# Kernel optimization log

Measured on AMD Instinct MI355X. Metric: run time of the kernel, lower is better.

## Reference

```python
import jax, jax.numpy as jnp
import numpy as np

CLAMP_MIN = -1.0
CLAMP_MAX = 1.0
EPS = 1e-5


def setup_inputs() -> dict:
    key = jax.random.key(0)
    k1, k2, k3, k4 = jax.random.split(key, 4)
    x = jax.random.normal(k1, (16, 3, 64, 64, 64), dtype=jnp.float32)
    w = jax.random.normal(k2, (16, 3, 3, 3, 3), dtype=jnp.float32) * 0.11  # ~kaiming scale for fan_in=81
    b = jax.random.normal(k3, (16,), dtype=jnp.float32) * 0.1
    m = jax.random.normal(k4, (16, 1, 1, 1), dtype=jnp.float32)
    return {"x": x, "w": w, "b": b, "m": m}


def reference(x, w, b, m):
    # Valid 3D conv: [N,3,D,H,W] x [16,3,3,3,3] -> [N,16,D-2,H-2,W-2]
    y = jax.lax.conv_general_dilated(
        x, w, window_strides=(1, 1, 1), padding='VALID',
        dimension_numbers=('NCDHW', 'OIDHW', 'NCDHW'))
    y = y + b[None, :, None, None, None]
    y = y * m[None]  # per-channel multiply before instance norm
    # InstanceNorm3d (affine=False, biased variance) over spatial dims per (n, c)
    mu = jnp.mean(y, axis=(2, 3, 4), keepdims=True)
    var = jnp.var(y, axis=(2, 3, 4), keepdims=True)
    y = (y - mu) * jax.lax.rsqrt(var + EPS)
    # clamp, second per-channel multiply, then max over channel dim
    y = jnp.clip(y, CLAMP_MIN, CLAMP_MAX) * m[None]
    return jnp.max(y, axis=1)  # [N, D-2, H-2, W-2]
```

## Files before the change

### kernel.cpp

```cpp
#include <hip/hip_runtime.h>
#include <hip/hip_bf16.h>
#include <float.h>

#define DI   64
#define DOUT 62
#define CI   3
#define CO   16
#define NB   16
constexpr int SP    = DOUT * DOUT * DOUT;
constexpr int SP64  = DOUT * DOUT * 64;
constexpr int HT    = 31;
constexpr int DT    = 16;
constexpr int NPART = HT * DT;
constexpr int XDW   = NB * CI * DI * DI * DI / 2;
constexpr int RSTR  = 34;
constexpr int PHD   = 72 * RSTR;

typedef __attribute__((ext_vector_type(8))) short bf16x8;
typedef __attribute__((ext_vector_type(4))) float f32x4;

__device__ float g_psum[NB * CO * NPART];
__device__ float g_psq [NB * CO * NPART];
__device__ float g_stats[NB * CO * 2];
__device__ uint4 g_wb4[4 * 64];
__device__ uint2 g_rt [4 * 64];
__device__ unsigned int g_xbf[XDW];

__device__ __forceinline__ unsigned short f2bf(float v) {
    __hip_bfloat16 h = __float2bfloat16(v);
    return __builtin_bit_cast(unsigned short, h);
}
__device__ __forceinline__ unsigned int pk2(float lo, float hi) {
    return (unsigned int)f2bf(lo) | ((unsigned int)f2bf(hi) << 16);
}

__global__ __launch_bounds__(256) void x2bf_kernel(const float* __restrict__ x)
{
    int i = blockIdx.x * 256 + threadIdx.x;
    const int stride = gridDim.x * 256;
    for (; i < XDW / 2; i += stride) {
        const float4 v = ((const float4*)x)[i];
        uint2 u;
        u.x = pk2(v.x, v.y);
        u.y = pk2(v.z, v.w);
        ((uint2*)g_xbf)[i] = u;
    }
}

__global__ void reorg_w_kernel(const float* __restrict__ w)
{
    unsigned int* dst = (unsigned int*)g_wb4;
    for (int dwi = threadIdx.x; dwi < 4 * 64 * 4; dwi += 256) {
        const int t    = dwi >> 8;
        const int lane = (dwi >> 2) & 63;
        const int dw   = dwi & 3;
        const int o    = lane & 15, q = lane >> 4;
        const int P    = t * 4 + q;
        unsigned int u = 0;
        for (int half = 0; half < 2; ++half) {
            const int j = dw * 2 + half;
            const int g = (j < 4) ? (2 * P) : (2 * P + 1);
            const int r = j & 3;
            float val = 0.f;
            if (g <= 26 && r < 3) {
                const int i = g / 9, kd = (g % 9) / 3, kh = g % 3;
                val = w[o * 81 + i * 27 + kd * 9 + kh * 3 + r];
            }
            u |= ((unsigned int)f2bf(val)) << (16 * half);
        }
        dst[dwi] = u;
    }
    if (threadIdx.x < 256) {
        const int t = threadIdx.x >> 6, lane = threadIdx.x & 63;
        const int q = lane >> 4, P = t * 4 + q;
        uint2 rt;
        const int gA = 2 * P, gB = 2 * P + 1;
        rt.x = (gA <= 26) ? ((gA / 9) * 24 + ((gA % 9) / 3) * 4 + gA % 3) * RSTR : 0;
        rt.y = (gB <= 26) ? ((gB / 9) * 24 + ((gB % 9) / 3) * 4 + gB % 3) * RSTR : 0;
        g_rt[t * 64 + lane] = rt;
    }
}

template <int MODE>
__global__ __launch_bounds__(512) void conv_mfma_kernel(
    const float* __restrict__ m,
    unsigned int* __restrict__ y32, float* __restrict__ out)
{
    __shared__ unsigned int xs[4 * PHD];
    __shared__ float redS[8][CO], redQ[8][CO];

    const int lane = threadIdx.x, ty = threadIdx.y;
    const int h0 = blockIdx.x * 2, d0 = blockIdx.y * 4, n = blockIdx.z;
    const int tid = ty * 64 + lane;

    for (int idx = tid; idx < 72 * 16; idx += 512) {
        const int row = idx >> 4, t = (idx & 15) * 2;
        const int i = row / 24, rm = row % 24, p = rm >> 2, hr = rm & 3;
        const int dg = min(d0 + p, DI - 1);
        const uint2 u = *(const uint2*)(g_xbf +
                          (((n * CI + i) * DI + dg) * DI + (h0 + hr)) * 32 + t);
        const unsigned D2 = __shfl_down(u.x, 1);
        const unsigned D3 = __shfl_down(u.y, 1);
        const unsigned a10 = __builtin_amdgcn_alignbit(u.y, u.x, 16);
        const unsigned a21 = __builtin_amdgcn_alignbit(D2, u.y, 16);
        const unsigned a32 = __builtin_amdgcn_alignbit(D3, D2, 16);
        unsigned int* dp = xs + row * RSTR + t;
        *(uint2*)(dp + 0 * PHD) = u;
        *(uint2*)(dp + 1 * PHD) = make_uint2(a10, a21);
        *(uint2*)(dp + 2 * PHD) = make_uint2(u.y, D2);
        *(uint2*)(dp + 3 * PHD) = make_uint2(a21, a32);
    }
    __syncthreads();

    const int c = lane & 15, q = lane >> 4;
    const int dl = ty >> 1, hl = ty & 1;
    const int offr = ((dl << 2) + hl) * RSTR;

    bf16x8 wf[4];
    int aA[4], aB[4];
#pragma unroll
    for (int t = 0; t < 4; ++t) {
        wf[t] = __builtin_bit_cast(bf16x8, g_wb4[t * 64 + lane]);
        const uint2 rt = g_rt[t * 64 + lane];
        aA[t] = (int)rt.x + offr + 2 * c;
        aB[t] = (int)rt.y + offr + 2 * c;
    }

    const float mc = m[c];
    float A = 0.f, Bp = 0.f;
    if (MODE == 2) {
        A  = g_stats[(n * CO + c) * 2 + 0];
        Bp = g_stats[(n * CO + c) * 2 + 1];
    }

    const int d = d0 + dl, h = h0 + hl;
    const bool dvalid = d < DOUT;
    float sS = 0.f, qS = 0.f;

    if (dvalid) {
        f32x4 acc[4];
#pragma unroll
        for (int wt = 0; wt < 4; ++wt) {
            f32x4 a = {0.f, 0.f, 0.f, 0.f};
#pragma unroll
            for (int t = 0; t < 4; ++t) {
                const uint2 lo = *(const uint2*)(xs + wt * PHD + aA[t]);
                const uint2 hi = *(const uint2*)(xs + wt * PHD + aB[t]);
                uint4 av;
                av.x = lo.x; av.y = lo.y; av.z = hi.x; av.w = hi.y;
                a = __builtin_amdgcn_mfma_f32_16x16x32_bf16(
                        __builtin_bit_cast(bf16x8, av), wf[t], a, 0, 0, 0);
            }
            acc[wt] = a;
        }

        if (MODE == 2) {
            const size_t spb = (size_t)(d * DOUT + h) * DOUT + 16 * q;
#pragma unroll
            for (int reg = 0; reg < 4; ++reg)
#pragma unroll
                for (int wt = 0; wt < 4; ++wt) {
                    const int p = reg * 4 + wt;
                    float z = fminf(fmaxf(fmaf(acc[wt][reg], A, Bp), -1.f), 1.f) * mc;
                    z = fmaxf(z, __shfl_xor(z, 1));
                    z = fmaxf(z, __shfl_xor(z, 2));
                    z = fmaxf(z, __shfl_xor(z, 4));
                    z = fmaxf(z, __shfl_xor(z, 8));
                    if (c == p && (p < 14 || q < 3))
                        out[(size_t)n * SP + spb + p] = z;
                }
        } else {
#pragma unroll
            for (int wt = 0; wt < 4; ++wt)
#pragma unroll
                for (int reg = 0; reg < 4; ++reg) {
                    float a = acc[wt][reg];
                    if ((wt >= 2) && (reg == 3)) a = (q < 3) ? a : 0.f;
                    sS += a; qS = fmaf(a, a, qS);
                }
            if (MODE == 1) {
                const size_t ypd = (size_t)(n * CO + c) * (SP64 / 2)
                                 + (size_t)(d * DOUT + h) * 32 + 8 * q;
                uint4 s0, s1;
                s0.x = pk2(acc[0][0], acc[1][0]); s0.y = pk2(acc[2][0], acc[3][0]);
                s0.z = pk2(acc[0][1], acc[1][1]); s0.w = pk2(acc[2][1], acc[3][1]);
                s1.x = pk2(acc[0][2], acc[1][2]); s1.y = pk2(acc[2][2], acc[3][2]);
                s1.z = pk2(acc[0][3], acc[1][3]); s1.w = pk2(acc[2][3], acc[3][3]);
                *(uint4*)(y32 + ypd)     = s0;
                *(uint4*)(y32 + ypd + 4) = s1;
            }
        }
    }

    if (MODE != 2) {
        sS += __shfl_xor(sS, 16); qS += __shfl_xor(qS, 16);
        sS += __shfl_xor(sS, 32); qS += __shfl_xor(qS, 32);
        if (lane < 16) { redS[ty][c] = sS; redQ[ty][c] = qS; }
        __syncthreads();
        if (ty == 0 && lane < 16) {
            float s = 0.f, qq = 0.f;
#pragma unroll
            for (int wv = 0; wv < 8; ++wv) { s += redS[wv][lane]; qq += redQ[wv][lane]; }
            const int blk = blockIdx.y * HT + blockIdx.x;
            g_psum[(n * CO + lane) * NPART + blk] = s;
            g_psq [(n * CO + lane) * NPART + blk] = qq;
        }
    }
}

__global__ __launch_bounds__(256) void finalize_stats_kernel(const float* __restrict__ m)
{
    const int idx = blockIdx.x;
    const int tid = threadIdx.x;
    __shared__ float ls[256], lq[256];
    float s = g_psum[idx * NPART + tid];
    float q = g_psq [idx * NPART + tid];
    if (tid + 256 < NPART) {
        s += g_psum[idx * NPART + tid + 256];
        q += g_psq [idx * NPART + tid + 256];
    }
    ls[tid] = s; lq[tid] = q;
    __syncthreads();
    for (int off = 128; off > 0; off >>= 1) {
        if (tid < off) { ls[tid] += ls[tid + off]; lq[tid] += lq[tid + off]; }
        __syncthreads();
    }
    if (tid == 0) {
        const float inv_n = 1.0f / (float)SP;
        const float muA = ls[0] * inv_n;
        const float varA = fmaxf(lq[0] * inv_n - muA * muA, 0.f);
        const float mo = m[idx & 15];
        const float isv = rsqrtf(fmaf(mo * mo, varA, 1e-5f));
        const float A = mo * isv;
        g_stats[idx * 2 + 0] = A;
        g_stats[idx * 2 + 1] = -muA * A;
    }
}

__global__ __launch_bounds__(256) void pass2_kernel(
    const unsigned int* __restrict__ y32, const float* __restrict__ m,
    float* __restrict__ out)
{
    const int n = blockIdx.y;
    const int t = blockIdx.x * 256 + threadIdx.x;
    if (t >= DOUT * DOUT * 32) return;
    const int wp = t & 31;
    if (wp == 31) return;
    const int row = t >> 5;
    const float* st = g_stats + n * CO * 2;
    const unsigned int* yn = y32 + (size_t)n * CO * (SP64 / 2) + t;
    float mx0 = -FLT_MAX, mx1 = -FLT_MAX;
#pragma unroll
    for (int o = 0; o < CO; ++o) {
        const unsigned int u = yn[(size_t)o * (SP64 / 2)];
        const float a0 = __uint_as_float(u << 16);
        const float a1 = __uint_as_float(u & 0xFFFF0000u);
        const float A = st[o * 2], Bp = st[o * 2 + 1], mo = m[o];
        const float z0 = fminf(fmaxf(fmaf(a0, A, Bp), -1.f), 1.f) * mo;
        const float z1 = fminf(fmaxf(fmaf(a1, A, Bp), -1.f), 1.f) * mo;
        mx0 = fmaxf(mx0, z0); mx1 = fmaxf(mx1, z1);
    }
    const int sp = row * DOUT + 2 * wp;
    *(float2*)(out + (size_t)n * SP + sp) = make_float2(mx0, mx1);
}

extern "C" void kernel_launch(void* const* d_in, const int* in_sizes, int n_in,
                              void* d_out, int out_size, void* d_ws, size_t ws_size,
                              hipStream_t stream)
{
    const float* x = (const float*)d_in[0];
    const float* w = (const float*)d_in[1];
    const float* m = (const float*)d_in[3];
    float* out = (float*)d_out;

    const dim3 blk(64, 8);
    const dim3 grd(HT, DT, NB);
    const size_t yBytes = (size_t)NB * CO * SP64 * 2;

    x2bf_kernel<<<dim3(2048), dim3(256), 0, stream>>>(x);
    reorg_w_kernel<<<dim3(1), dim3(256), 0, stream>>>(w);

    if (ws_size >= yBytes) {
        unsigned int* y = (unsigned int*)d_ws;
        conv_mfma_kernel<1><<<grd, blk, 0, stream>>>(m, y, nullptr);
        finalize_stats_kernel<<<dim3(NB * CO), dim3(256), 0, stream>>>(m);
        pass2_kernel<<<dim3((DOUT * DOUT * 32 + 255) / 256, NB), dim3(256), 0, stream>>>(y, m, out);
    } else {
        conv_mfma_kernel<0><<<grd, blk, 0, stream>>>(m, nullptr, nullptr);
        finalize_stats_kernel<<<dim3(NB * CO), dim3(256), 0, stream>>>(m);
        conv_mfma_kernel<2><<<grd, blk, 0, stream>>>(m, nullptr, out);
    }
}
```

Baseline: 93.60 us.

## Fuse weight reorg into x conversion, widen pass2 loads, tweak LDS stride

```diff
diff --git a/kernel.cpp b/kernel.cpp
--- a/kernel.cpp
+++ b/kernel.cpp
@@ -13,7 +13,7 @@
 constexpr int DT    = 16;
 constexpr int NPART = HT * DT;
 constexpr int XDW   = NB * CI * DI * DI * DI / 2;
-constexpr int RSTR  = 34;
+constexpr int RSTR  = 33;
 constexpr int PHD   = 72 * RSTR;
 
 typedef __attribute__((ext_vector_type(8))) short bf16x8;
@@ -34,8 +34,41 @@
     return (unsigned int)f2bf(lo) | ((unsigned int)f2bf(hi) << 16);
 }
 
-__global__ __launch_bounds__(256) void x2bf_kernel(const float* __restrict__ x)
-{
+__global__ __launch_bounds__(256) void x2bf_kernel(const float* __restrict__ x,
+                                                   const float* __restrict__ w)
+{
+    if (blockIdx.x == 0) {
+        unsigned int* dst = (unsigned int*)g_wb4;
+        for (int dwi = threadIdx.x; dwi < 4 * 64 * 4; dwi += 256) {
+            const int t    = dwi >> 8;
+            const int lane = (dwi >> 2) & 63;
+            const int dw   = dwi & 3;
+            const int o    = lane & 15, q = lane >> 4;
+            const int P    = t * 4 + q;
+            unsigned int u = 0;
+            for (int half = 0; half < 2; ++half) {
+                const int j = dw * 2 + half;
+                const int g = (j < 4) ? (2 * P) : (2 * P + 1);
+                const int r = j & 3;
+                float val = 0.f;
+                if (g <= 26 && r < 3) {
+                    const int i = g / 9, kd = (g % 9) / 3, kh = g % 3;
+                    val = w[o * 81 + i * 27 + kd * 9 + kh * 3 + r];
+                }
+                u |= ((unsigned int)f2bf(val)) << (16 * half);
+            }
+            dst[dwi] = u;
+        }
+        if (threadIdx.x < 256) {
+            const int t = threadIdx.x >> 6, lane = threadIdx.x & 63;
+            const int q = lane >> 4, P = t * 4 + q;
+            uint2 rt;
+            const int gA = 2 * P, gB = 2 * P + 1;
+            rt.x = (gA <= 26) ? ((gA / 9) * 24 + ((gA % 9) / 3) * 4 + gA % 3) * RSTR : 0;
+            rt.y = (gB <= 26) ? ((gB / 9) * 24 + ((gB % 9) / 3) * 4 + gB % 3) * RSTR : 0;
+            g_rt[t * 64 + lane] = rt;
+        }
+    }
     int i = blockIdx.x * 256 + threadIdx.x;
     const int stride = gridDim.x * 256;
     for (; i < XDW / 2; i += stride) {
@@ -44,40 +77,6 @@
         u.x = pk2(v.x, v.y);
         u.y = pk2(v.z, v.w);
         ((uint2*)g_xbf)[i] = u;
-    }
-}
-
-__global__ void reorg_w_kernel(const float* __restrict__ w)
-{
-    unsigned int* dst = (unsigned int*)g_wb4;
-    for (int dwi = threadIdx.x; dwi < 4 * 64 * 4; dwi += 256) {
-        const int t    = dwi >> 8;
-        const int lane = (dwi >> 2) & 63;
-        const int dw   = dwi & 3;
-        const int o    = lane & 15, q = lane >> 4;
-        const int P    = t * 4 + q;
-        unsigned int u = 0;
-        for (int half = 0; half < 2; ++half) {
-            const int j = dw * 2 + half;
-            const int g = (j < 4) ? (2 * P) : (2 * P + 1);
-            const int r = j & 3;
-            float val = 0.f;
-            if (g <= 26 && r < 3) {
-                const int i = g / 9, kd = (g % 9) / 3, kh = g % 3;
-                val = w[o * 81 + i * 27 + kd * 9 + kh * 3 + r];
-            }
-            u |= ((unsigned int)f2bf(val)) << (16 * half);
-        }
-        dst[dwi] = u;
-    }
-    if (threadIdx.x < 256) {
-        const int t = threadIdx.x >> 6, lane = threadIdx.x & 63;
-        const int q = lane >> 4, P = t * 4 + q;
-        uint2 rt;
-        const int gA = 2 * P, gB = 2 * P + 1;
-        rt.x = (gA <= 26) ? ((gA / 9) * 24 + ((gA % 9) / 3) * 4 + gA % 3) * RSTR : 0;
-        rt.y = (gB <= 26) ? ((gB / 9) * 24 + ((gB % 9) / 3) * 4 + gB % 3) * RSTR : 0;
-        g_rt[t * 64 + lane] = rt;
     }
 }
 
@@ -174,10 +173,14 @@
             for (int wt = 0; wt < 4; ++wt)
 #pragma unroll
                 for (int reg = 0; reg < 4; ++reg) {
-                    float a = acc[wt][reg];
-                    if ((wt >= 2) && (reg == 3)) a = (q < 3) ? a : 0.f;
+                    const float a = acc[wt][reg];
                     sS += a; qS = fmaf(a, a, qS);
                 }
+            if (q == 3) {
+                const float e2 = acc[2][3], e3 = acc[3][3];
+                sS -= e2 + e3;
+                qS -= fmaf(e2, e2, e3 * e3);
+            }
             if (MODE == 1) {
                 const size_t ypd = (size_t)(n * CO + c) * (SP64 / 2)
                                  + (size_t)(d * DOUT + h) * 32 + 8 * q;
@@ -242,26 +245,30 @@
     float* __restrict__ out)
 {
     const int n = blockIdx.y;
-    const int t = blockIdx.x * 256 + threadIdx.x;
-    if (t >= DOUT * DOUT * 32) return;
-    const int wp = t & 31;
-    if (wp == 31) return;
-    const int row = t >> 5;
+    const int t2 = blockIdx.x * 256 + threadIdx.x;
+    if (t2 >= DOUT * DOUT * 16) return;
+    const int wp2 = t2 & 15;
+    const int row = t2 >> 4;
     const float* st = g_stats + n * CO * 2;
-    const unsigned int* yn = y32 + (size_t)n * CO * (SP64 / 2) + t;
-    float mx0 = -FLT_MAX, mx1 = -FLT_MAX;
+    const uint2* yn = (const uint2*)(y32 + (size_t)n * CO * (SP64 / 2)) + t2 + row * 0;
+    float mx0 = -FLT_MAX, mx1 = -FLT_MAX, mx2 = -FLT_MAX, mx3 = -FLT_MAX;
 #pragma unroll
     for (int o = 0; o < CO; ++o) {
-        const unsigned int u = yn[(size_t)o * (SP64 / 2)];
-        const float a0 = __uint_as_float(u << 16);
-        const float a1 = __uint_as_float(u & 0xFFFF0000u);
+        const uint2 u = yn[(size_t)o * (SP64 / 4)];
         const float A = st[o * 2], Bp = st[o * 2 + 1], mo = m[o];
-        const float z0 = fminf(fmaxf(fmaf(a0, A, Bp), -1.f), 1.f) * mo;
-        const float z1 = fminf(fmaxf(fmaf(a1, A, Bp), -1.f), 1.f) * mo;
-        mx0 = fmaxf(mx0, z0); mx1 = fmaxf(mx1, z1);
-    }
-    const int sp = row * DOUT + 2 * wp;
-    *(float2*)(out + (size_t)n * SP + sp) = make_float2(mx0, mx1);
+        float z;
+        z = fminf(fmaxf(fmaf(__uint_as_float(u.x << 16),         A, Bp), -1.f), 1.f) * mo;
+        mx0 = fmaxf(mx0, z);
+        z = fminf(fmaxf(fmaf(__uint_as_float(u.x & 0xFFFF0000u), A, Bp), -1.f), 1.f) * mo;
+        mx1 = fmaxf(mx1, z);
+        z = fminf(fmaxf(fmaf(__uint_as_float(u.y << 16),         A, Bp), -1.f), 1.f) * mo;
+        mx2 = fmaxf(mx2, z);
+        z = fminf(fmaxf(fmaf(__uint_as_float(u.y & 0xFFFF0000u), A, Bp), -1.f), 1.f) * mo;
+        mx3 = fmaxf(mx3, z);
+    }
+    float* op = out + (size_t)n * SP + (size_t)row * DOUT + 4 * wp2;
+    *(float2*)op = make_float2(mx0, mx1);
+    if (wp2 < 15) *(float2*)(op + 2) = make_float2(mx2, mx3);
 }
 
 extern "C" void kernel_launch(void* const* d_in, const int* in_sizes, int n_in,
@@ -277,14 +284,13 @@
     const dim3 grd(HT, DT, NB);
     const size_t yBytes = (size_t)NB * CO * SP64 * 2;
 
-    x2bf_kernel<<<dim3(2048), dim3(256), 0, stream>>>(x);
-    reorg_w_kernel<<<dim3(1), dim3(256), 0, stream>>>(w);
+    x2bf_kernel<<<dim3(2048), dim3(256), 0, stream>>>(x, w);
 
     if (ws_size >= yBytes) {
         unsigned int* y = (unsigned int*)d_ws;
         conv_mfma_kernel<1><<<grd, blk, 0, stream>>>(m, y, nullptr);
         finalize_stats_kernel<<<dim3(NB * CO), dim3(256), 0, stream>>>(m);
-        pass2_kernel<<<dim3((DOUT * DOUT * 32 + 255) / 256, NB), dim3(256), 0, stream>>>(y, m, out);
+        pass2_kernel<<<dim3((DOUT * DOUT * 16 + 255) / 256, NB), dim3(256), 0, stream>>>(y, m, out);
     } else {
         conv_mfma_kernel<0><<<grd, blk, 0, stream>>>(m, nullptr, nullptr);
         finalize_stats_kernel<<<dim3(NB * CO), dim3(256), 0, stream>>>(m);
```

New measurement: 104.4 us. 11.5% more time.
